# Kernel tuning notes

Hardware: AMD Instinct MI355X
Metric: run time of the kernel (lower is better)

The kernel has to match this reference:

```python
import jax, jax.numpy as jnp
import numpy as np

B, N, DIM, H = 2, 4096, 1024, 16
LAT = 1024
CTX = N - LAT            # 3072 context tokens
SEG = 12                 # num_segments
CHUNK = CTX // SEG       # 256 tokens per segment
D = DIM // H             # 64 head dim
SCALE = D ** -0.5
LN_EPS = 1e-5
NEG = float(-np.finfo(np.float32).max)


def _split_heads(t):  # [B, N, DIM] -> [(B*H), N, D]
    return t.reshape(B, N, H, D).transpose(0, 2, 1, 3).reshape(B * H, N, D)


def _merge_heads(t):  # [(B*H), n, D] -> [B, n, DIM]
    n = t.shape[1]
    return t.reshape(B, H, n, D).transpose(0, 2, 1, 3).reshape(B, n, DIM)


def _layernorm(t, g, b):  # LN over last dim (head dim)
    mu = t.mean(-1, keepdims=True)
    var = ((t - mu) ** 2).mean(-1, keepdims=True)
    return (t - mu) * jax.lax.rsqrt(var + LN_EPS) * g + b


def _rope(t):  # rotary embedding over full head dim, half-split rotate
    pos = jnp.arange(N, dtype=jnp.float32)
    inv = 1.0 / (10000.0 ** (jnp.arange(0, D, 2, dtype=jnp.float32) / D))
    freqs = pos[:, None] * inv[None, :]          # [N, D/2]
    emb = jnp.concatenate([freqs, freqs], -1)    # [N, D]
    cos, sin = jnp.cos(emb), jnp.sin(emb)
    rot = jnp.concatenate([-t[..., D // 2:], t[..., : D // 2]], -1)
    return t * cos + rot * sin


def setup_inputs() -> dict:
    key = jax.random.key(0)
    ks = jax.random.split(key, 4)
    s = 0.02
    return {
        "x": jax.random.normal(ks[0], (B, N, DIM), jnp.float32),
        "Wq": jax.random.normal(ks[1], (DIM, DIM), jnp.float32) * s,
        "Wkv": jax.random.normal(ks[2], (DIM, DIM), jnp.float32) * s,
        "Wo": jax.random.normal(ks[3], (DIM, DIM), jnp.float32) * s,
        "bo": jnp.zeros((DIM,), jnp.float32),
        "ln_g": jnp.ones((D,), jnp.float32),
        "ln_b": jnp.zeros((D,), jnp.float32),
    }


def reference(x, Wq, Wkv, Wo, bo, ln_g, ln_b):
    q = _split_heads(x @ Wq)    # [(BH), N, D]
    kv = _split_heads(x @ Wkv)  # [(BH), N, D]
    q, kv = _rope(q), _rope(kv)

    lkv = _layernorm(kv, ln_g, ln_b)  # normalized keys/values, full seq

    q_lat = q[:, CTX:] * SCALE                                   # [(BH), LAT, D]
    q_ctx = (q[:, :CTX] * SCALE).reshape(B * H, SEG, CHUNK, D)   # segmented ctx queries
    lkv_ctx = lkv[:, :CTX].reshape(B * H, SEG, CHUNK, D)         # segmented norm'd kv

    # latent queries: full attention over all N positions, causal among latents
    lsim = jnp.einsum('bid,bjd->bij', q_lat, lkv)                # [(BH), LAT, N]
    tri = jnp.triu(jnp.ones((LAT, LAT), bool), 1)
    lat_block = jnp.where(tri, NEG, lsim[:, :, CTX:])
    lsim = jnp.concatenate([lsim[:, :, :CTX], lat_block], axis=-1)
    attn = jax.nn.softmax(lsim, axis=-1)
    out_lat = jnp.einsum('bij,bjd->bid', attn, lkv)              # [(BH), LAT, D]

    # context queries: block-diagonal segmented local attention (non-causal)
    sim_ctx = jnp.einsum('bsid,bsjd->bsij', q_ctx, lkv_ctx)      # [(BH), SEG, CHUNK, CHUNK]
    attn_ctx = jax.nn.softmax(sim_ctx, axis=-1)
    out_ctx = jnp.einsum('bsij,bsjd->bsid', attn_ctx, lkv_ctx).reshape(B * H, CTX, D)

    out = jnp.concatenate([_merge_heads(out_ctx), _merge_heads(out_lat)], axis=1)
    return out @ Wo + bo
```

## Files before the change

kernel.cpp:

```cpp
#include <hip/hip_runtime.h>
#include <math.h>

#define NB_B 2
#define NB_N 4096
#define NB_DIM 1024
#define NB_H 16
#define NB_D 64
#define NB_CTX 3072
#define NSPLIT 4
#define QSCALE 0.18033688011112042f
#define NEGF -3.0e38f

typedef __attribute__((ext_vector_type(8))) short short8;
typedef __attribute__((ext_vector_type(4))) short s4v;
typedef __attribute__((ext_vector_type(4))) float f32x4;
typedef __fp16 fp16x2 __attribute__((ext_vector_type(2)));

#if __has_builtin(__builtin_amdgcn_mfma_f32_16x16x16bf16_1k)
__device__ __forceinline__ f32x4 mfma16(s4v a, s4v b, f32x4 c) {
  return __builtin_amdgcn_mfma_f32_16x16x16bf16_1k(a, b, c, 0, 0, 0);
}
#else
__device__ __forceinline__ f32x4 mfma16(s4v a, s4v b, f32x4 c) {
  f32x4 d;
  asm volatile("v_mfma_f32_16x16x16_bf16 %0, %1, %2, %3"
               : "=v"(d) : "v"(a), "v"(b), "v"(c));
  return d;
}
#endif

__device__ __forceinline__ unsigned short f2bf(float f) {
  union { float f; unsigned u; } v; v.f = f;
  unsigned r = v.u + 0x7fffu + ((v.u >> 16) & 1u);
  return (unsigned short)(r >> 16);
}

__device__ __forceinline__ unsigned int cvtpk(float a, float b) {
  unsigned int r;
  asm("v_cvt_pk_bf16_f32 %0, %1, %2" : "=v"(r) : "v"(a), "v"(b));
  return r;
}

__device__ __forceinline__ unsigned int pkh(float a, float b) {
  union { fp16x2 h; unsigned int u; } cv;
  cv.h = __builtin_amdgcn_cvt_pkrtz(a, b);
  return cv.u;
}

__device__ __forceinline__ void async16(const void* g, void* l) {
  typedef const unsigned int __attribute__((address_space(1)))* gas_t;
  typedef unsigned int __attribute__((address_space(3)))* las_t;
  __builtin_amdgcn_global_load_lds((gas_t)(unsigned long long)g,
                                   (las_t)(unsigned)(unsigned long long)l,
                                   16, 0, 0);
}

__global__ __launch_bounds__(256) void k_prep(
    const float* __restrict__ x,
    const float* __restrict__ Wq, const float* __restrict__ Wkv, const float* __restrict__ Wo,
    unsigned short* __restrict__ xb, unsigned short* __restrict__ WqkvT,
    unsigned short* __restrict__ WoT, float2* __restrict__ tab)
{
  __shared__ float tile[64][65];
  const int bx = blockIdx.x, tid = threadIdx.x;
  if (bx < 2048) {
    const float4* x4 = (const float4*)x;
    ushort4* xb4 = (ushort4*)xb;
    const int n4 = (NB_B * NB_N * NB_DIM) / 4;
    for (int i = bx * 256 + tid; i < n4; i += 2048 * 256) {
      float4 v = x4[i];
      ushort4 o;
      o.x = f2bf(v.x); o.y = f2bf(v.y); o.z = f2bf(v.z); o.w = f2bf(v.w);
      xb4[i] = o;
    }
  } else if (bx < 2816) {
    int idx = bx - 2048;
    int z = idx >> 8, rem = idx & 255;
    const float* W; unsigned short* out;
    if (z == 0)      { W = Wq;  out = WqkvT; }
    else if (z == 1) { W = Wkv; out = WqkvT + 1024 * 1024; }
    else             { W = Wo;  out = WoT; }
    int c0 = (rem & 15) * 64, k0 = (rem >> 4) * 64;
    int tx = tid & 63, ty = tid >> 6;
    #pragma unroll
    for (int i = 0; i < 16; ++i) {
      int k = ty + i * 4;
      tile[k][tx] = W[(long)(k0 + k) * 1024 + c0 + tx];
    }
    __syncthreads();
    #pragma unroll
    for (int i = 0; i < 16; ++i) {
      int c = ty + i * 4;
      out[(long)(c0 + c) * 1024 + k0 + tx] = f2bf(tile[tx][c]);
    }
  } else {
    int idx = (bx - 2816) * 256 + tid;
    int n = idx >> 5, fi = idx & 31;
    float inv = exp2f(-(float)fi * (13.287712379549449f / 32.0f));
    float ang = (float)n * inv;
    float s, c;
    sincosf(ang, &s, &c);
    tab[idx] = make_float2(c, s);
  }
}

__global__ __launch_bounds__(256) void k_gemm_qkv(
    const unsigned short* __restrict__ A,
    const unsigned short* __restrict__ Bt,
    unsigned short* __restrict__ qf,
    unsigned short* __restrict__ lkvp,
    const float2* __restrict__ tab,
    const float* __restrict__ ln_g,
    const float* __restrict__ ln_b)
{
  __shared__ unsigned short As[2][128 * 32];
  __shared__ unsigned short Bs[2][128 * 32];
  const int tid = threadIdx.x;
  const int w = tid >> 6, lane = tid & 63;
  const int wr = w >> 1, wc = w & 1;
  const int quad = lane >> 4, l15 = lane & 15;
  const long tm = (long)blockIdx.y * 128, tn = (long)blockIdx.x * 128;
  const int K = 1024;

  f32x4 acc[4][4];
  #pragma unroll
  for (int i = 0; i < 4; ++i)
    #pragma unroll
    for (int j = 0; j < 4; ++j)
      acc[i][j] = (f32x4){0.f, 0.f, 0.f, 0.f};

  const unsigned short* Ag0 = A + (tm + w * 16 + (lane >> 2)) * K + (lane & 3) * 8;
  const unsigned short* Bg0 = Bt + (tn + w * 16 + (lane >> 2)) * K + (lane & 3) * 8;
  const unsigned short* Ag1 = Ag0 + (long)64 * K;
  const unsigned short* Bg1 = Bg0 + (long)64 * K;
  unsigned short* Al0 = &As[0][(w * 16) * 32];
  unsigned short* Al1 = &As[0][(64 + w * 16) * 32];
  unsigned short* Bl0 = &Bs[0][(w * 16) * 32];
  unsigned short* Bl1 = &Bs[0][(64 + w * 16) * 32];
  unsigned short* Ah0 = &As[1][(w * 16) * 32];
  unsigned short* Ah1 = &As[1][(64 + w * 16) * 32];
  unsigned short* Bh0 = &Bs[1][(w * 16) * 32];
  unsigned short* Bh1 = &Bs[1][(64 + w * 16) * 32];

  for (int k0 = 0; k0 < K; k0 += 64) {
    __syncthreads();
    async16(Ag0 + k0, Al0);      async16(Ag0 + k0 + 32, Ah0);
    async16(Ag1 + k0, Al1);      async16(Ag1 + k0 + 32, Ah1);
    async16(Bg0 + k0, Bl0);      async16(Bg0 + k0 + 32, Bh0);
    async16(Bg1 + k0, Bl1);      async16(Bg1 + k0 + 32, Bh1);
    __syncthreads();
    #pragma unroll
    for (int h = 0; h < 2; ++h) {
      short8 af[4], bfr[4];
      #pragma unroll
      for (int i = 0; i < 4; ++i)
        af[i] = *(const short8*)&As[h][(wr * 64 + i * 16 + l15) * 32 + quad * 8];
      #pragma unroll
      for (int j = 0; j < 4; ++j)
        bfr[j] = *(const short8*)&Bs[h][(wc * 64 + j * 16 + l15) * 32 + quad * 8];
      #pragma unroll
      for (int i = 0; i < 4; ++i)
        #pragma unroll
        for (int j = 0; j < 4; ++j)
          acc[i][j] = __builtin_amdgcn_mfma_f32_16x16x32_bf16(af[i], bfr[j], acc[i][j], 0, 0, 0);
    }
  }

  const int col_base = (int)tn + wc * 64;
  const bool is_q = col_base < 1024;
  const int hh = (col_base & 1023) >> 6;
  unsigned short* dst = is_q ? qf : lkvp;
  float g_ln[4], b_ln[4];
  #pragma unroll
  for (int j = 0; j < 4; ++j) { g_ln[j] = ln_g[j * 16 + l15]; b_ln[j] = ln_b[j * 16 + l15]; }

  const int row_base = (int)tm + wr * 64;
  #pragma unroll
  for (int i = 0; i < 4; ++i) {
    #pragma unroll
    for (int r = 0; r < 4; ++r) {
      const int row = row_base + i * 16 + quad * 4 + r;
      const int n = row & 4095, b = row >> 12;
      const float2 cs0 = tab[n * 32 + l15];
      const float2 cs1 = tab[n * 32 + 16 + l15];
      float val[4];
      #pragma unroll
      for (int j = 0; j < 4; ++j) {
        float t = acc[i][j][r], pt = acc[i][j ^ 2][r];
        float2 cs = (j & 1) ? cs1 : cs0;
        float rot = (j < 2) ? -pt : pt;
        val[j] = t * cs.x + rot * cs.y;
      }
      unsigned short* orow = dst + ((long)(b * 16 + hh) * NB_N + n) * 64;
      if (is_q) {
        #pragma unroll
        for (int j = 0; j < 4; ++j)
          orow[j * 16 + l15] = f2bf(val[j] * QSCALE);
      } else {
        float s = val[0] + val[1] + val[2] + val[3];
        #pragma unroll
        for (int o = 1; o < 16; o <<= 1) s += __shfl_xor(s, o);
        const float mu = s * 0.015625f;
        float dv[4], vs = 0.f;
        #pragma unroll
        for (int j = 0; j < 4; ++j) { dv[j] = val[j] - mu; vs += dv[j] * dv[j]; }
        #pragma unroll
        for (int o = 1; o < 16; o <<= 1) vs += __shfl_xor(vs, o);
        const float rr = rsqrtf(vs * 0.015625f + 1e-5f);
        #pragma unroll
        for (int j = 0; j < 4; ++j)
          orow[j * 16 + l15] = f2bf(dv[j] * rr * g_ln[j] + b_ln[j]);
      }
    }
  }
}

__global__ __launch_bounds__(256) void k_gemm_bt(
    const unsigned short* __restrict__ A,
    const unsigned short* __restrict__ Bt,
    float* __restrict__ C,
    const float* __restrict__ bias,
    int K, int ldc)
{
  __shared__ unsigned short As[2][128 * 32];
  __shared__ unsigned short Bs[2][128 * 32];
  const int tid = threadIdx.x;
  const int w = tid >> 6, lane = tid & 63;
  const int wr = w >> 1, wc = w & 1;
  const int quad = lane >> 4, l15 = lane & 15;
  const long tm = (long)blockIdx.y * 128, tn = (long)blockIdx.x * 128;

  f32x4 acc[4][4];
  #pragma unroll
  for (int i = 0; i < 4; ++i)
    #pragma unroll
    for (int j = 0; j < 4; ++j)
      acc[i][j] = (f32x4){0.f, 0.f, 0.f, 0.f};

  const unsigned short* Ag0 = A + (tm + w * 16 + (lane >> 2)) * K + (lane & 3) * 8;
  const unsigned short* Bg0 = Bt + (tn + w * 16 + (lane >> 2)) * K + (lane & 3) * 8;
  const unsigned short* Ag1 = Ag0 + (long)64 * K;
  const unsigned short* Bg1 = Bg0 + (long)64 * K;
  unsigned short* Al0 = &As[0][(w * 16) * 32];
  unsigned short* Al1 = &As[0][(64 + w * 16) * 32];
  unsigned short* Bl0 = &Bs[0][(w * 16) * 32];
  unsigned short* Bl1 = &Bs[0][(64 + w * 16) * 32];
  unsigned short* Ah0 = &As[1][(w * 16) * 32];
  unsigned short* Ah1 = &As[1][(64 + w * 16) * 32];
  unsigned short* Bh0 = &Bs[1][(w * 16) * 32];
  unsigned short* Bh1 = &Bs[1][(64 + w * 16) * 32];

  for (int k0 = 0; k0 < K; k0 += 64) {
    __syncthreads();
    async16(Ag0 + k0, Al0);      async16(Ag0 + k0 + 32, Ah0);
    async16(Ag1 + k0, Al1);      async16(Ag1 + k0 + 32, Ah1);
    async16(Bg0 + k0, Bl0);      async16(Bg0 + k0 + 32, Bh0);
    async16(Bg1 + k0, Bl1);      async16(Bg1 + k0 + 32, Bh1);
    __syncthreads();
    #pragma unroll
    for (int h = 0; h < 2; ++h) {
      short8 af[4], bfr[4];
      #pragma unroll
      for (int i = 0; i < 4; ++i)
        af[i] = *(const short8*)&As[h][(wr * 64 + i * 16 + l15) * 32 + quad * 8];
      #pragma unroll
      for (int j = 0; j < 4; ++j)
        bfr[j] = *(const short8*)&Bs[h][(wc * 64 + j * 16 + l15) * 32 + quad * 8];
      #pragma unroll
      for (int i = 0; i < 4; ++i)
        #pragma unroll
        for (int j = 0; j < 4; ++j)
          acc[i][j] = __builtin_amdgcn_mfma_f32_16x16x32_bf16(af[i], bfr[j], acc[i][j], 0, 0, 0);
    }
  }

  #pragma unroll
  for (int j = 0; j < 4; ++j) {
    const long col = tn + wc * 64 + j * 16 + l15;
    const float bv = bias ? bias[col] : 0.0f;
    #pragma unroll
    for (int i = 0; i < 4; ++i) {
      #pragma unroll
      for (int r = 0; r < 4; ++r) {
        const long row = tm + wr * 64 + i * 16 + quad * 4 + r;
        C[row * ldc + col] = acc[i][j][r] + bv;
      }
    }
  }
}


__device__ __forceinline__ void stage_kv(
    unsigned short* __restrict__ Ksn, unsigned short* __restrict__ Vtn,
    const int kp, const int sdc, const uint4& gA, const uint4& gB)
{
  *(uint4*)&Ksn[(2 * kp) * 72 + sdc * 8] = gA;
  *(uint4*)&Ksn[(2 * kp + 1) * 72 + sdc * 8] = gB;
  const unsigned int* wA = (const unsigned int*)&gA;
  const unsigned int* wB = (const unsigned int*)&gB;
  #pragma unroll
  for (int jw = 0; jw < 4; ++jw) {
    const unsigned int lo = __builtin_amdgcn_perm(wB[jw], wA[jw], 0x05040100u);
    const unsigned int hi = __builtin_amdgcn_perm(wB[jw], wA[jw], 0x07060302u);
    const int d0 = sdc * 8 + jw * 2;
    const int xo = (2 * kp) ^ (d0 & 56);
    *(unsigned int*)&Vtn[d0 * 72 + xo] = lo;
    *(unsigned int*)&Vtn[(d0 + 1) * 72 + xo] = hi;
  }
}

#define NB_PACK(QG, SUB)                                               \
  _Pragma("unroll")                                                    \
  for (int k4 = 0; k4 < 4; ++k4) {                                     \
    const float p0 = __builtin_amdgcn_exp2f(st[QG][k4][0] SUB);        \
    const float p1 = __builtin_amdgcn_exp2f(st[QG][k4][1] SUB);        \
    const float p2 = __builtin_amdgcn_exp2f(st[QG][k4][2] SUB);        \
    const float p3 = __builtin_amdgcn_exp2f(st[QG][k4][3] SUB);        \
    pk[QG][k4][0] = cvtpk(p0, p1);                                     \
    pk[QG][k4][1] = cvtpk(p2, p3);                                     \
  }

__device__ __forceinline__ void attn_tile(
    const unsigned short* __restrict__ Ks, const unsigned short* __restrict__ Vt,
    unsigned short* __restrict__ Ksn, unsigned short* __restrict__ Vtn,
    const int kt, const int kt1, const int kstart, const bool latent, const int q0lat,
    const int w, const int quad, const int l15, const int kp, const int sdc,
    const unsigned short* __restrict__ kbase,
    uint4& gA, uint4& gB, const short8 (&qfr)[2][2],
    f32x4 (&ot)[2][4], f32x4 (&lacc)[2], float& miu, float& thr)
{
  const int key0 = kstart + kt * 64;
  __syncthreads();

  if (kt + 1 < kt1) {
    stage_kv(Ksn, Vtn, kp, sdc, gA, gB);
    if (kt + 2 < kt1) {
      const long k2 = (long)(key0 + 128);
      gA = *(const uint4*)(kbase + (k2 + 2 * kp) * 64 + sdc * 8);
      gB = *(const uint4*)(kbase + (k2 + 2 * kp + 1) * 64 + sdc * 8);
    }
  }

  f32x4 st[2][4];
  #pragma unroll
  for (int qg = 0; qg < 2; ++qg)
    #pragma unroll
    for (int k4 = 0; k4 < 4; ++k4)
      st[qg][k4] = (f32x4){0.f, 0.f, 0.f, 0.f};
  __builtin_amdgcn_s_setprio(1);
  #pragma unroll
  for (int kc = 0; kc < 2; ++kc) {
    short8 kf[4];
    #pragma unroll
    for (int k4 = 0; k4 < 4; ++k4)
      kf[k4] = *(const short8*)&Ks[(k4 * 16 + l15) * 72 + kc * 32 + quad * 8];
    #pragma unroll
    for (int qg = 0; qg < 2; ++qg)
      #pragma unroll
      for (int k4 = 0; k4 < 4; ++k4)
        st[qg][k4] = __builtin_amdgcn_mfma_f32_16x16x32_bf16(kf[k4], qfr[qg][kc], st[qg][k4], 0, 0, 0);
  }
  __builtin_amdgcn_s_setprio(0);

  if (latent && key0 + 63 >= NB_CTX) {
    #pragma unroll
    for (int qg = 0; qg < 2; ++qg) {
      const int qrow = q0lat + w * 32 + qg * 16 + l15;
      #pragma unroll
      for (int k4 = 0; k4 < 4; ++k4)
        #pragma unroll
        for (int r = 0; r < 4; ++r) {
          const int kl = key0 + k4 * 16 + quad * 4 + r - NB_CTX;
          if (kl > qrow) st[qg][k4][r] = NEGF;
        }
    }
  }

  float mx = st[0][0][0];
  #pragma unroll
  for (int qg = 0; qg < 2; ++qg)
    #pragma unroll
    for (int k4 = 0; k4 < 4; ++k4)
      mx = fmaxf(mx, fmaxf(fmaxf(st[qg][k4][0], st[qg][k4][1]),
                           fmaxf(st[qg][k4][2], st[qg][k4][3])));

  unsigned int pk[2][4][2];
  if (miu == 0.f) {
    NB_PACK(0, )
    NB_PACK(1, )
  } else {
    NB_PACK(0, - miu)
    NB_PACK(1, - miu)
  }

  const s4v vones = { (short)0x3F80, (short)0x3F80, (short)0x3F80, (short)0x3F80 };
  __builtin_amdgcn_s_setprio(1);
  #pragma unroll
  for (int k4 = 0; k4 < 4; ++k4) {
    s4v vf[4];
    const int kb = k4 * 16 + quad * 4;
    #pragma unroll
    for (int dt = 0; dt < 4; ++dt) {
      const int row = dt * 16 + l15;
      vf[dt] = *(const s4v*)&Vt[row * 72 + (kb ^ (row & 56))];
    }
    #pragma unroll
    for (int qg = 0; qg < 2; ++qg) {
      s4v pf;
      ((unsigned int*)&pf)[0] = pk[qg][k4][0];
      ((unsigned int*)&pf)[1] = pk[qg][k4][1];
      lacc[qg] = mfma16(vones, pf, lacc[qg]);
      #pragma unroll
      for (int dt = 0; dt < 4; ++dt)
        ot[qg][dt] = mfma16(vf[dt], pf, ot[qg][dt]);
    }
  }
  __builtin_amdgcn_s_setprio(0);

  if (__builtin_expect(__any(mx > thr), 0)) {
    #pragma unroll
    for (int o = 1; o < 64; o <<= 1) mx = fmaxf(mx, __shfl_xor(mx, o));
    const float c = __builtin_amdgcn_exp2f(miu - mx);
    miu = mx; thr = mx + 8.f;
    #pragma unroll
    for (int qg = 0; qg < 2; ++qg) {
      lacc[qg][0] *= c; lacc[qg][1] *= c; lacc[qg][2] *= c; lacc[qg][3] *= c;
      #pragma unroll
      for (int dt = 0; dt < 4; ++dt) {
        ot[qg][dt][0] *= c; ot[qg][dt][1] *= c;
        ot[qg][dt][2] *= c; ot[qg][dt][3] *= c;
      }
    }
  }
}

__global__ __launch_bounds__(256) void k_attn(
    const unsigned short* __restrict__ qf,
    const unsigned short* __restrict__ lkv,
    unsigned short* __restrict__ attn_out,
    unsigned short* __restrict__ Opart,
    float* __restrict__ mpart,
    float* __restrict__ lpart)
{
  __shared__ unsigned short smem[18432];
  unsigned short* const Ks0 = smem;
  unsigned short* const Vt0 = smem + 4608;
  unsigned short* const Ks1 = smem + 9216;
  unsigned short* const Vt1 = smem + 13824;

  const int tid = threadIdx.x;
  const int w = tid >> 6, lane = tid & 63;
  const int quad = lane >> 4, l15 = lane & 15;

  const int bx = blockIdx.x;
  int bh, q0tok, kstart, kt0, kt1, q0lat, s6 = 0, qb = 0;
  bool latent;
  if (bx < 256 * NSPLIT) {
    latent = true;
    qb = bx / NSPLIT;
    s6 = bx % NSPLIT;
    bh = qb >> 3;
    q0lat = (qb & 7) * 128;
    q0tok = NB_CTX + q0lat;
    kstart = 0;
    const int nkt = (NB_CTX + q0lat + 128) >> 6;
    const int hk = nkt >> 1;
    kt0 = 2 * ((s6 * hk) / NSPLIT);
    kt1 = 2 * (((s6 + 1) * hk) / NSPLIT);
  } else {
    latent = false;
    int idx = bx - 256 * NSPLIT;
    bh = idx / 24;
    int r2 = idx % 24;
    int seg = r2 >> 1;
    q0lat = 0;
    q0tok = seg * 256 + (r2 & 1) * 128;
    kstart = seg * 256;
    kt0 = 0; kt1 = 4;
  }

  const unsigned short* qbase = qf + ((long)bh * NB_N + q0tok) * 64;
  const unsigned short* kbase = lkv + (long)bh * NB_N * 64;

  short8 qfr[2][2];
  #pragma unroll
  for (int qg = 0; qg < 2; ++qg)
    #pragma unroll
    for (int kc = 0; kc < 2; ++kc)
      qfr[qg][kc] = *(const short8*)(qbase + (w * 32 + qg * 16 + l15) * 64 + kc * 32 + quad * 8);

  const int kp = tid >> 3, sdc = tid & 7;

  uint4 gA, gB;
  {
    const int key0 = kstart + kt0 * 64;
    gA = *(const uint4*)(kbase + (long)(key0 + 2 * kp) * 64 + sdc * 8);
    gB = *(const uint4*)(kbase + (long)(key0 + 2 * kp + 1) * 64 + sdc * 8);
  }
  stage_kv(Ks0, Vt0, kp, sdc, gA, gB);
  {
    const int key1 = kstart + (kt0 + 1) * 64;
    gA = *(const uint4*)(kbase + (long)(key1 + 2 * kp) * 64 + sdc * 8);
    gB = *(const uint4*)(kbase + (long)(key1 + 2 * kp + 1) * 64 + sdc * 8);
  }

  f32x4 ot[2][4];
  f32x4 lacc[2];
  float miu = 0.f, thr = 8.f;
  #pragma unroll
  for (int qg = 0; qg < 2; ++qg) {
    #pragma unroll
    for (int dt = 0; dt < 4; ++dt) ot[qg][dt] = (f32x4){0.f, 0.f, 0.f, 0.f};
    lacc[qg] = (f32x4){0.f, 0.f, 0.f, 0.f};
  }

  for (int kt = kt0; kt < kt1; kt += 2) {
    attn_tile(Ks0, Vt0, Ks1, Vt1, kt,     kt1, kstart, latent, q0lat,
              w, quad, l15, kp, sdc, kbase, gA, gB, qfr, ot, lacc, miu, thr);
    attn_tile(Ks1, Vt1, Ks0, Vt0, kt + 1, kt1, kstart, latent, q0lat,
              w, quad, l15, kp, sdc, kbase, gA, gB, qfr, ot, lacc, miu, thr);
  }

  __syncthreads();
  if (latent) {
    const long pb = (long)(s6 * 256 + qb);
    if (quad == 0) {
      #pragma unroll
      for (int qg = 0; qg < 2; ++qg) {
        mpart[pb * 128 + w * 32 + qg * 16 + l15] = miu;
        lpart[pb * 128 + w * 32 + qg * 16 + l15] = lacc[qg][0];
      }
    }
    unsigned short* obase = Opart + pb * 8192;
    #pragma unroll
    for (int qg = 0; qg < 2; ++qg) {
      const float inv = 1.0f / lacc[qg][0];
      const int q = w * 32 + qg * 16 + l15;
      #pragma unroll
      for (int dt = 0; dt < 4; ++dt) {
        uint2 u;
        u.x = pkh(ot[qg][dt][0] * inv, ot[qg][dt][1] * inv);
        u.y = pkh(ot[qg][dt][2] * inv, ot[qg][dt][3] * inv);
        *(uint2*)&obase[q * 64 + dt * 16 + quad * 4] = u;
      }
    }
  } else {
    #pragma unroll
    for (int qg = 0; qg < 2; ++qg) {
      const float inv = 1.0f / lacc[qg][0];
      const int q = w * 32 + qg * 16 + l15;
      #pragma unroll
      for (int dt = 0; dt < 4; ++dt)
        #pragma unroll
        for (int r = 0; r < 4; ++r)
          smem[q * 72 + dt * 16 + quad * 4 + r] = f2bf(ot[qg][dt][r] * inv);
    }
    __syncthreads();
    const int qrow = tid >> 1, half = tid & 1;
    const int b_ = bh >> 4, h_ = bh & 15;
    unsigned short* orow = attn_out + ((long)b_ * NB_N + q0tok + qrow) * NB_DIM + h_ * 64 + half * 32;
    #pragma unroll
    for (int v = 0; v < 4; ++v)
      *(uint4*)(orow + v * 8) = *(const uint4*)&smem[qrow * 72 + half * 32 + v * 8];
  }
}

__global__ __launch_bounds__(256) void k_combine(
    const unsigned short* __restrict__ Opart, const float* __restrict__ mpart,
    const float* __restrict__ lpart, unsigned short* __restrict__ attn_out)
{
  const int qb = blockIdx.x;
  const int bh = qb >> 3, qt = qb & 7;
  const int b = bh >> 4, h = bh & 15;
  const int t = threadIdx.x;
  const int q = t >> 1;
  const int dh = (t & 1) * 32;

  float m[NSPLIT], l[NSPLIT], mstar = NEGF;
  #pragma unroll
  for (int s = 0; s < NSPLIT; ++s) {
    m[s] = mpart[(s * 256 + qb) * 128 + q];
    l[s] = lpart[(s * 256 + qb) * 128 + q];
    mstar = fmaxf(mstar, m[s]);
  }
  float wsum = 0.f, ws[NSPLIT];
  #pragma unroll
  for (int s = 0; s < NSPLIT; ++s) {
    ws[s] = __builtin_amdgcn_exp2f(m[s] - mstar) * l[s];
    wsum += ws[s];
  }
  const float inv = 1.0f / wsum;

  float acc[32];
  #pragma unroll
  for (int d = 0; d < 32; ++d) acc[d] = 0.f;

  #pragma unroll
  for (int s = 0; s < NSPLIT; ++s) {
    const unsigned short* base = Opart + ((long)(s * 256 + qb)) * 8192 + q * 64 + dh;
    const float wv = ws[s];
    #pragma unroll
    for (int v = 0; v < 4; ++v) {
      uint4 u = *(const uint4*)(base + v * 8);
      const unsigned int uw[4] = {u.x, u.y, u.z, u.w};
      #pragma unroll
      for (int e = 0; e < 4; ++e) {
        union { unsigned int u; fp16x2 h; } cv; cv.u = uw[e];
        acc[v * 8 + e * 2]     += wv * (float)cv.h[0];
        acc[v * 8 + e * 2 + 1] += wv * (float)cv.h[1];
      }
    }
  }

  unsigned short* orow = attn_out + ((long)b * NB_N + NB_CTX + qt * 128 + q) * NB_DIM + h * 64 + dh;
  #pragma unroll
  for (int v = 0; v < 4; ++v) {
    uint4 u;
    u.x = (unsigned)f2bf(acc[v * 8 + 0] * inv) | ((unsigned)f2bf(acc[v * 8 + 1] * inv) << 16);
    u.y = (unsigned)f2bf(acc[v * 8 + 2] * inv) | ((unsigned)f2bf(acc[v * 8 + 3] * inv) << 16);
    u.z = (unsigned)f2bf(acc[v * 8 + 4] * inv) | ((unsigned)f2bf(acc[v * 8 + 5] * inv) << 16);
    u.w = (unsigned)f2bf(acc[v * 8 + 6] * inv) | ((unsigned)f2bf(acc[v * 8 + 7] * inv) << 16);
    *(uint4*)(orow + v * 8) = u;
  }
}

extern "C" void kernel_launch(void* const* d_in, const int* in_sizes, int n_in,
                              void* d_out, int out_size, void* d_ws, size_t ws_size,
                              hipStream_t stream)
{
  const float* x    = (const float*)d_in[0];
  const float* Wq   = (const float*)d_in[1];
  const float* Wkv  = (const float*)d_in[2];
  const float* Wo   = (const float*)d_in[3];
  const float* bo   = (const float*)d_in[4];
  const float* ln_g = (const float*)d_in[5];
  const float* ln_b = (const float*)d_in[6];
  float* out = (float*)d_out;

  char* ws = (char*)d_ws;
  unsigned short* xb    = (unsigned short*)(ws);
  unsigned short* WqkvT = (unsigned short*)(ws + (size_t)(16 << 20));
  unsigned short* WoT   = (unsigned short*)(ws + (size_t)(20 << 20));
  float2*         tab   = (float2*)        (ws + (size_t)(22 << 20));
  unsigned short* qfb   = (unsigned short*)(ws + (size_t)(24 << 20));
  unsigned short* lkv   = (unsigned short*)(ws + (size_t)(40 << 20));
  unsigned short* aout  = (unsigned short*)(ws + (size_t)(56 << 20));
  unsigned short* Opart = (unsigned short*)(ws + (size_t)(72 << 20));
  float*          mpart = (float*)         (ws + (size_t)(112 << 20));
  float*          lpart = (float*)         (ws + (size_t)(113 << 20));

  hipLaunchKernelGGL(k_prep, dim3(3328), dim3(256), 0, stream,
                     x, Wq, Wkv, Wo, xb, WqkvT, WoT, tab);
  hipLaunchKernelGGL(k_gemm_qkv, dim3(16, 64), dim3(256), 0, stream,
                     xb, WqkvT, qfb, lkv, tab, ln_g, ln_b);
  hipLaunchKernelGGL(k_attn, dim3(256 * NSPLIT + 768), dim3(256), 0, stream,
                     qfb, lkv, aout, Opart, mpart, lpart);
  hipLaunchKernelGGL(k_combine, dim3(256), dim3(256), 0, stream,
                     Opart, mpart, lpart, aout);
  hipLaunchKernelGGL(k_gemm_bt, dim3(8, 64), dim3(256), 0, stream,
                     aout, WoT, out, bo, 1024, 1024);
}
```

Baseline: 277.1 us.

## Double-buffer GEMM k-loop so async LDS loads overlap MFMA compute

Both bf16 GEMM kernels (the fused QKV projection and the output projection) now split the 64-wide k-step into two 32-wide LDS buffers. Each buffer is prefetched with async global-to-LDS loads while the MFMAs consume the other buffer, instead of loading both halves and then computing. MFMA sections are also wrapped in s_setprio to favour the math waves. The aim is to hide global-load latency behind tensor-core work. In exchange, each tile carries less work per barrier and the number of barriers per k-step stays the same.

```diff
diff --git a/kernel.cpp b/kernel.cpp
--- a/kernel.cpp
+++ b/kernel.cpp
@@ -133,37 +133,41 @@
   const unsigned short* Bg0 = Bt + (tn + w * 16 + (lane >> 2)) * K + (lane & 3) * 8;
   const unsigned short* Ag1 = Ag0 + (long)64 * K;
   const unsigned short* Bg1 = Bg0 + (long)64 * K;
-  unsigned short* Al0 = &As[0][(w * 16) * 32];
-  unsigned short* Al1 = &As[0][(64 + w * 16) * 32];
-  unsigned short* Bl0 = &Bs[0][(w * 16) * 32];
-  unsigned short* Bl1 = &Bs[0][(64 + w * 16) * 32];
-  unsigned short* Ah0 = &As[1][(w * 16) * 32];
-  unsigned short* Ah1 = &As[1][(64 + w * 16) * 32];
-  unsigned short* Bh0 = &Bs[1][(w * 16) * 32];
-  unsigned short* Bh1 = &Bs[1][(64 + w * 16) * 32];
-
+  const int so0 = (w * 16) * 32;
+  const int so1 = (64 + w * 16) * 32;
+
+#define QKV_STAGE(b, k)                         \
+  async16(Ag0 + (k), &As[b][so0]);              \
+  async16(Ag1 + (k), &As[b][so1]);              \
+  async16(Bg0 + (k), &Bs[b][so0]);              \
+  async16(Bg1 + (k), &Bs[b][so1]);
+
+#define QKV_CONSUME(b)                                                          \
+  {                                                                             \
+    short8 af[4], bfr[4];                                                       \
+    _Pragma("unroll")                                                           \
+    for (int i = 0; i < 4; ++i)                                                 \
+      af[i] = *(const short8*)&As[b][(wr * 64 + i * 16 + l15) * 32 + quad * 8]; \
+    _Pragma("unroll")                                                           \
+    for (int j = 0; j < 4; ++j)                                                 \
+      bfr[j] = *(const short8*)&Bs[b][(wc * 64 + j * 16 + l15) * 32 + quad * 8];\
+    __builtin_amdgcn_s_setprio(1);                                              \
+    _Pragma("unroll")                                                           \
+    for (int i = 0; i < 4; ++i)                                                 \
+      _Pragma("unroll")                                                         \
+      for (int j = 0; j < 4; ++j)                                               \
+        acc[i][j] = __builtin_amdgcn_mfma_f32_16x16x32_bf16(af[i], bfr[j], acc[i][j], 0, 0, 0); \
+    __builtin_amdgcn_s_setprio(0);                                              \
+  }
+
+  QKV_STAGE(0, 0);
   for (int k0 = 0; k0 < K; k0 += 64) {
     __syncthreads();
-    async16(Ag0 + k0, Al0);      async16(Ag0 + k0 + 32, Ah0);
-    async16(Ag1 + k0, Al1);      async16(Ag1 + k0 + 32, Ah1);
-    async16(Bg0 + k0, Bl0);      async16(Bg0 + k0 + 32, Bh0);
-    async16(Bg1 + k0, Bl1);      async16(Bg1 + k0 + 32, Bh1);
+    if (k0 + 32 < K) { QKV_STAGE(1, k0 + 32); }
+    QKV_CONSUME(0);
     __syncthreads();
-    #pragma unroll
-    for (int h = 0; h < 2; ++h) {
-      short8 af[4], bfr[4];
-      #pragma unroll
-      for (int i = 0; i < 4; ++i)
-        af[i] = *(const short8*)&As[h][(wr * 64 + i * 16 + l15) * 32 + quad * 8];
-      #pragma unroll
-      for (int j = 0; j < 4; ++j)
-        bfr[j] = *(const short8*)&Bs[h][(wc * 64 + j * 16 + l15) * 32 + quad * 8];
-      #pragma unroll
-      for (int i = 0; i < 4; ++i)
-        #pragma unroll
-        for (int j = 0; j < 4; ++j)
-          acc[i][j] = __builtin_amdgcn_mfma_f32_16x16x32_bf16(af[i], bfr[j], acc[i][j], 0, 0, 0);
-    }
+    if (k0 + 64 < K) { QKV_STAGE(0, k0 + 64); }
+    QKV_CONSUME(1);
   }
 
   const int col_base = (int)tn + wc * 64;
@@ -241,37 +245,17 @@
   const unsigned short* Bg0 = Bt + (tn + w * 16 + (lane >> 2)) * K + (lane & 3) * 8;
   const unsigned short* Ag1 = Ag0 + (long)64 * K;
   const unsigned short* Bg1 = Bg0 + (long)64 * K;
-  unsigned short* Al0 = &As[0][(w * 16) * 32];
-  unsigned short* Al1 = &As[0][(64 + w * 16) * 32];
-  unsigned short* Bl0 = &Bs[0][(w * 16) * 32];
-  unsigned short* Bl1 = &Bs[0][(64 + w * 16) * 32];
-  unsigned short* Ah0 = &As[1][(w * 16) * 32];
-  unsigned short* Ah1 = &As[1][(64 + w * 16) * 32];
-  unsigned short* Bh0 = &Bs[1][(w * 16) * 32];
-  unsigned short* Bh1 = &Bs[1][(64 + w * 16) * 32];
-
+  const int so0 = (w * 16) * 32;
+  const int so1 = (64 + w * 16) * 32;
+
+  QKV_STAGE(0, 0);
   for (int k0 = 0; k0 < K; k0 += 64) {
     __syncthreads();
-    async16(Ag0 + k0, Al0);      async16(Ag0 + k0 + 32, Ah0);
-    async16(Ag1 + k0, Al1);      async16(Ag1 + k0 + 32, Ah1);
-    async16(Bg0 + k0, Bl0);      async16(Bg0 + k0 + 32, Bh0);
-    async16(Bg1 + k0, Bl1);      async16(Bg1 + k0 + 32, Bh1);
+    if (k0 + 32 < K) { QKV_STAGE(1, k0 + 32); }
+    QKV_CONSUME(0);
     __syncthreads();
-    #pragma unroll
-    for (int h = 0; h < 2; ++h) {
-      short8 af[4], bfr[4];
-      #pragma unroll
-      for (int i = 0; i < 4; ++i)
-        af[i] = *(const short8*)&As[h][(wr * 64 + i * 16 + l15) * 32 + quad * 8];
-      #pragma unroll
-      for (int j = 0; j < 4; ++j)
-        bfr[j] = *(const short8*)&Bs[h][(wc * 64 + j * 16 + l15) * 32 + quad * 8];
-      #pragma unroll
-      for (int i = 0; i < 4; ++i)
-        #pragma unroll
-        for (int j = 0; j < 4; ++j)
-          acc[i][j] = __builtin_amdgcn_mfma_f32_16x16x32_bf16(af[i], bfr[j], acc[i][j], 0, 0, 0);
-    }
+    if (k0 + 64 < K) { QKV_STAGE(0, k0 + 64); }
+    QKV_CONSUME(1);
   }
 
   #pragma unroll
```

Result: faster. 257.9 us (-6.9%).
